# Kernel tuning notes

Hardware: AMD Instinct MI355X
Metric: run time of the kernel (lower is better)

The kernel has to match this reference:

```python
import jax, jax.numpy as jnp
import numpy as np

T, B, IN, H, L = 1024, 128, 100, 200, 2


def _lstm_layer(x, h0, c0, W_ih, W_hh, b_ih, b_hh):
    # x: [T, B, in]; h0, c0: [B, H]; W_ih: [4H, in]; W_hh: [4H, H]
    # PyTorch gate order: i, f, g, o
    def step(carry, x_t):
        h, c = carry
        gates = x_t @ W_ih.T + b_ih + h @ W_hh.T + b_hh  # [B, 4H]
        i, f, g, o = jnp.split(gates, 4, axis=-1)
        i = jax.nn.sigmoid(i)
        f = jax.nn.sigmoid(f)
        g = jnp.tanh(g)
        o = jax.nn.sigmoid(o)
        c = f * c + i * g
        h = o * jnp.tanh(c)
        return (h, c), h

    (hT, cT), ys = jax.lax.scan(step, (h0, c0), x)
    return ys, hT, cT  # ys: [T, B, H]


def setup_inputs() -> dict:
    key = jax.random.key(0)
    ks = jax.random.split(key, 12)
    s = 1.0 / np.sqrt(H)  # PyTorch LSTM init scale
    return {
        "inp": jax.random.normal(ks[0], (T, B, IN), dtype=jnp.float32),
        "h0": jnp.zeros((L, B, H), dtype=jnp.float32),
        "c0": jnp.zeros((L, B, H), dtype=jnp.float32),
        "W_ih0": jax.random.uniform(ks[1], (4 * H, IN), jnp.float32, -s, s),
        "W_hh0": jax.random.uniform(ks[2], (4 * H, H), jnp.float32, -s, s),
        "b_ih0": jax.random.uniform(ks[3], (4 * H,), jnp.float32, -s, s),
        "b_hh0": jax.random.uniform(ks[4], (4 * H,), jnp.float32, -s, s),
        "W_ih1": jax.random.uniform(ks[5], (4 * H, H), jnp.float32, -s, s),
        "W_hh1": jax.random.uniform(ks[6], (4 * H, H), jnp.float32, -s, s),
        "b_ih1": jax.random.uniform(ks[7], (4 * H,), jnp.float32, -s, s),
        "b_hh1": jax.random.uniform(ks[8], (4 * H,), jnp.float32, -s, s),
        "fc_W": jax.random.uniform(ks[9], (IN, H), jnp.float32, -s, s),
        "fc_b": jax.random.uniform(ks[10], (IN,), jnp.float32, -s, s),
    }


def reference(inp, h0, c0, W_ih0, W_hh0, b_ih0, b_hh0, W_ih1, W_hh1, b_ih1, b_hh1, fc_W, fc_b):
    # 2-layer LSTM (eval mode: inter-layer dropout is identity) + linear head
    y0, h0T, c0T = _lstm_layer(inp, h0[0], c0[0], W_ih0, W_hh0, b_ih0, b_hh0)
    y1, h1T, c1T = _lstm_layer(y0, h0[1], c0[1], W_ih1, W_hh1, b_ih1, b_hh1)
    output = y1 @ fc_W.T + fc_b  # [T, B, num_classes]
    hn = jnp.stack([h0T, h1T], axis=0)  # [2, B, H]
    cn = jnp.stack([c0T, c1T], axis=0)
    return output, hn, cn
```

## Files before the change

### kernel.cpp

```cpp
#include <hip/hip_runtime.h>
#include <stdint.h>

#define T_ 1024
#define B_ 128
#define IN_ 100
#define H_ 200
#define RD 8
#define RDY 8

typedef unsigned short u16;
typedef unsigned long long u64;
typedef short bf16x8 __attribute__((ext_vector_type(8)));
typedef float f32x4  __attribute__((ext_vector_type(4)));

#define OFF_Y1    0u
#define OFF_Y0R   52428800u
#define OFF_PR0   53248000u
#define OFF_PR1A  56524800u
#define OFF_PR1B  59801600u
#define OFF_PACK  63078400u
#define OFF_CBF   64409600u
#define OFF_CH0   65576256u
#define OFF_CC0   65781056u
#define OFF_X0P   65985856u
#define OFF_Y0P   65985920u
#define OFF_CONS0 65985984u
#define OFF_CONS1 65986048u
#define OFF_C1X   65986112u
#define OFF_Y0C   66018880u
#define OFF_FLAG  66051648u
#define WS_NEEDED 66051712u
#define PK_WHH0 0
#define PK_WHH1 179200
#define PK_WIH0 358400
#define PK_WIH1 460800

__device__ __forceinline__ float bf2f(u16 u) {
    union { uint32_t i; float f; } v; v.i = ((uint32_t)u) << 16; return v.f;
}
__device__ __forceinline__ u16 f2bf(float f) {
    union { uint32_t i; float f; } v; v.f = f;
    uint32_t x = v.i;
    x += 0x7fff + ((x >> 16) & 1);
    return (u16)(x >> 16);
}
__device__ __forceinline__ void agst2(float* p, float a, float b) {
    union { u64 u; float f[2]; } v; v.f[0] = a; v.f[1] = b;
    __hip_atomic_store((u64*)p, v.u, __ATOMIC_RELAXED, __HIP_MEMORY_SCOPE_AGENT);
}
__device__ __forceinline__ float2 agld2(const float* p) {
    union { u64 u; float f[2]; } v;
    v.u = __hip_atomic_load((u64*)p, __ATOMIC_RELAXED, __HIP_MEMORY_SCOPE_AGENT);
    return make_float2(v.f[0], v.f[1]);
}
__device__ __forceinline__ void agsti(int* p, int v) {
    __hip_atomic_store(p, v, __ATOMIC_RELAXED, __HIP_MEMORY_SCOPE_AGENT);
}
__device__ __forceinline__ void spin_ge(int* p, int val, int* budget) {
    while (__hip_atomic_load(p, __ATOMIC_RELAXED, __HIP_MEMORY_SCOPE_AGENT) < val) {
        __builtin_amdgcn_s_sleep(1);
        if (--(*budget) < 0) return;
    }
}

__global__ void detect_kernel(const void* w, int* flag) {
    __shared__ int cnt;
    if (threadIdx.x == 0) cnt = 0;
    __syncthreads();
    const u16* p = (const u16*)w;
    int bad = 0;
    for (int e = 0; e < 16; ++e) {
        u16 u = p[threadIdx.x * 16 + e];
        int ex = (u >> 7) & 0xFF;
        float v = bf2f(u);
        float av = v < 0.f ? -v : v;
        if (ex == 0xFF || av > 0.5f) bad++;
    }
    atomicAdd(&cnt, bad);
    __syncthreads();
    if (threadIdx.x == 0) flag[0] = (cnt > 64) ? 1 : 0;
}

__global__ void prep_kernel(const void* Wih0, const void* Whh0,
                            const void* bih0, const void* bhh0,
                            const void* Wih1, const void* Whh1,
                            const void* bih1, const void* bhh1,
                            const void* fcW,  const void* fcb,
                            const void* h0,   const void* c0,
                            u16* cbf, float* ch0, float* cc0, const int* flag)
{
    const int isf32 = *flag;
    const int N = 685700;
    for (int idx = blockIdx.x * 256 + threadIdx.x; idx < N; idx += gridDim.x * 256) {
        const void* src; int e = idx; u16* du = nullptr; float* df = nullptr;
        if (e < 80000)                 { src = Wih0; du = cbf; }
        else if ((e -= 80000) < 160000){ src = Whh0; du = cbf + 80000; }
        else if ((e -= 160000) < 800)  { src = bih0; du = cbf + 240000; }
        else if ((e -= 800) < 800)     { src = bhh0; du = cbf + 240800; }
        else if ((e -= 800) < 160000)  { src = Wih1; du = cbf + 241600; }
        else if ((e -= 160000) < 160000){ src = Whh1; du = cbf + 401600; }
        else if ((e -= 160000) < 800)  { src = bih1; du = cbf + 561600; }
        else if ((e -= 800) < 800)     { src = bhh1; du = cbf + 562400; }
        else if ((e -= 800) < 20000)   { src = fcW;  du = cbf + 563200; }
        else if ((e -= 20000) < 100)   { src = fcb;  du = cbf + 583200; }
        else if ((e -= 100) < 51200)   { src = h0;   df = ch0; }
        else         { e -= 51200;       src = c0;   df = cc0; }
        float v = isf32 ? ((const float*)src)[e] : bf2f(((const u16*)src)[e]);
        if (du) du[e] = f2bf(v); else df[e] = v;
    }
}

__global__ void pack_kernel(const u16* __restrict__ cbf, u16* __restrict__ pw) {
    const int N = 665600;
    for (int idx = blockIdx.x * 256 + threadIdx.x; idx < N; idx += gridDim.x * 256) {
        int e = idx; const u16* src; int ld, koff, kmax, rel;
        if (e < 179200)                    { rel = e; src = cbf + 80000;  ld = 200; kmax = 200; koff = 0; }
        else if ((e -= 179200) < 179200)   { rel = e; src = cbf + 401600; ld = 200; kmax = 200; koff = 0; }
        else if ((e -= 179200) < 102400)   { rel = e; src = cbf + 0;      ld = 100; kmax = 100; koff = 0; }
        else { e -= 102400; const int kh = e / 102400; rel = e % 102400;
               src = cbf + 241600; ld = 200; kmax = 100; koff = kh * 100; }
        const int el = rel & 7, l = (rel >> 3) & 63, tile = rel >> 9;
        const int nt = tile % 50, kt = tile / 50;
        const int rp = nt * 16 + (l & 15), g = rp & 3, hc = rp >> 2;
        const int k = kt * 32 + ((l >> 4) << 3) + el;
        u16 v = 0;
        if (k < kmax) v = src[(g * 200 + hc) * ld + koff + k];
        pw[idx] = v;
    }
}

__launch_bounds__(512, 1)
__global__ void lstm_pipe(const void* __restrict__ inp, char* __restrict__ ws,
                          const int* __restrict__ flag, void* __restrict__ out)
{
    __shared__ __align__(16) u16 smem[67392];

    u16*   y1buf  = (u16*)(ws + OFF_Y1);
    float* y0ring = (float*)(ws + OFF_Y0R);
    float* pr0    = (float*)(ws + OFF_PR0);
    float* pr1a   = (float*)(ws + OFF_PR1A);
    float* pr1b   = (float*)(ws + OFF_PR1B);
    u16*   packs  = (u16*)(ws + OFF_PACK);
    const u16* cbf = (const u16*)(ws + OFF_CBF);
    const float* ch0 = (const float*)(ws + OFF_CH0);
    const float* cc0 = (const float*)(ws + OFF_CC0);
    int* x0prod = (int*)(ws + OFF_X0P);
    int* y0prod = (int*)(ws + OFF_Y0P);
    int* cons0  = (int*)(ws + OFF_CONS0);
    int* cons1  = (int*)(ws + OFF_CONS1);
    int* c1x    = (int*)(ws + OFF_C1X);
    int* y0c    = (int*)(ws + OFF_Y0C);

    const int isf32 = *flag;
    const int tid = threadIdx.x;
    const int bid = blockIdx.x;
    const int lane = tid & 63, wv = tid >> 6;
    const int lm = lane & 15, lq = lane >> 4;
    const int nslot = (wv < 2) ? 7 : 6;
    int budget = 1 << 22;

    if (bid < 16) {
        const int L = bid >> 3, i = bid & 7, b0 = i * 16;
        u16* ldsB = smem;
        u16* hls  = smem + 31744;
        float* gls = (float*)(smem + 40192);
        const u16* packW = packs + (L ? PK_WHH1 : PK_WHH0);

        bf16x8 Bv[36];
        #pragma unroll
        for (int s = 0; s < 7; ++s) {
            const int nt = (s < 6) ? (wv + 8 * s) : (48 + wv);
            #pragma unroll
            for (int kt = 0; kt < 7; ++kt) {
                if (s < 5) {
                    Bv[s * 7 + kt] = *(const bf16x8*)(packW + ((size_t)(kt * 50 + nt) * 64 + lane) * 8);
                } else if (s == 5 && kt == 0) {
                    Bv[35] = *(const bf16x8*)(packW + ((size_t)(kt * 50 + nt) * 64 + lane) * 8);
                }
            }
        }
        for (int u = tid; u < 31744; u += 512) {
            const int eidx = u >> 9, off = u & 511;
            int kt, nt;
            if (eidx < 48) { kt = 1 + eidx % 6; nt = (eidx / 6) + 40; }
            else { const int e2 = eidx - 48; kt = e2 % 7; nt = 48 + e2 / 7; }
            ldsB[u] = packW[(size_t)(kt * 50 + nt) * 512 + off];
        }
        for (int u = tid; u < 2 * 16 * 264; u += 512) {
            const int pl = u / (16 * 264), m = (u / 264) % 16, k = u % 264;
            u16 v = 0;
            if (k < 200) {
                const float h = ch0[L * B_ * H_ + (b0 + m) * H_ + k];
                const u16 hi = f2bf(h);
                v = pl ? f2bf(h - bf2f(hi)) : hi;
            }
            hls[u] = v;
        }
        float c2[4][2];
        #pragma unroll
        for (int k4 = 0; k4 < 4; ++k4) {
            const int p = tid + 512 * k4;
            c2[k4][0] = 0.f; c2[k4][1] = 0.f;
            if (p < 1600) {
                const int m = p / 100, hc = (p % 100) * 2;
                c2[k4][0] = cc0[L * B_ * H_ + (b0 + m) * H_ + hc];
                c2[k4][1] = cc0[L * B_ * H_ + (b0 + m) * H_ + hc + 1];
            }
        }
        f32x4 acc[7];
        if (tid == 0) {
            if (L == 0) spin_ge(x0prod + i, 1, &budget);
            else        spin_ge(c1x + i, 2, &budget);
        }
        __syncthreads();
        {
            const size_t roff = (size_t)(0 * 8 + i) * 12800;
            #pragma unroll
            for (int s = 0; s < 7; ++s) if (s < nslot) {
                const int nt = (s < 6) ? (wv + 8 * s) : (48 + wv);
                float* pa = ((L ? pr1a : pr0) + roff) + nt * 256 + lane * 4;
                const float2 a01 = agld2(pa);
                const float2 a23 = agld2(pa + 2);
                acc[s][0] = a01.x; acc[s][1] = a01.y;
                acc[s][2] = a23.x; acc[s][3] = a23.y;
                if (L) {
                    float* pb = (pr1b + roff) + nt * 256 + lane * 4;
                    const float2 b01 = agld2(pb);
                    const float2 b23 = agld2(pb + 2);
                    acc[s][0] += b01.x; acc[s][1] += b01.y;
                    acc[s][2] += b23.x; acc[s][3] += b23.y;
                }
            }
        }
        __syncthreads();

        for (int t = 0; t < T_; ++t) {
            #pragma unroll
            for (int kt = 0; kt < 7; ++kt) {
                const int ha = lm * 264 + kt * 32 + 8 * lq;
                const bf16x8 Ahi = *(const bf16x8*)(hls + ha);
                const bf16x8 Alo = *(const bf16x8*)(hls + 16 * 264 + ha);
                #pragma unroll
                for (int s = 0; s < 7; ++s) if (s < nslot) {
                    bf16x8 Bt;
                    if (s < 5)                 Bt = Bv[s * 7 + kt];
                    else if (s == 5 && kt == 0) Bt = Bv[35];
                    else {
                        const int eidx = (s == 5) ? (wv * 6 + kt - 1) : (48 + wv * 7 + kt);
                        Bt = *(const bf16x8*)(ldsB + eidx * 512 + lane * 8);
                    }
                    acc[s] = __builtin_amdgcn_mfma_f32_16x16x32_bf16(Ahi, Bt, acc[s], 0, 0, 0);
                    acc[s] = __builtin_amdgcn_mfma_f32_16x16x32_bf16(Alo, Bt, acc[s], 0, 0, 0);
                }
            }
            #pragma unroll
            for (int s = 0; s < 7; ++s) if (s < nslot) {
                const int nt = (s < 6) ? (wv + 8 * s) : (48 + wv);
                const int g = lm & 3, hc = nt * 4 + (lm >> 2);
                float* gp = gls + g * 3400 + hc * 17 + 4 * lq;
                gp[0] = acc[s][0]; gp[1] = acc[s][1]; gp[2] = acc[s][2]; gp[3] = acc[s][3];
            }
            __syncthreads();
            if (tid == 0) {
                if (t < T_ - 1) {
                    if (L == 0) spin_ge(x0prod + i, t + 2, &budget);
                    else        spin_ge(c1x + (t + 1) * 8 + i, 2, &budget);
                }
                if (L == 0 && t >= RDY) spin_ge(y0c + (t - RDY) * 8 + i, 2, &budget);
            }
            __syncthreads();
            if (t < T_ - 1) {
                const size_t roff = (size_t)(((t + 1) & (RD - 1)) * 8 + i) * 12800;
                #pragma unroll
                for (int s = 0; s < 7; ++s) if (s < nslot) {
                    const int nt = (s < 6) ? (wv + 8 * s) : (48 + wv);
                    float* pa = ((L ? pr1a : pr0) + roff) + nt * 256 + lane * 4;
                    const float2 a01 = agld2(pa);
                    const float2 a23 = agld2(pa + 2);
                    acc[s][0] = a01.x; acc[s][1] = a01.y;
                    acc[s][2] = a23.x; acc[s][3] = a23.y;
                    if (L) {
                        float* pb = (pr1b + roff) + nt * 256 + lane * 4;
                        const float2 b01 = agld2(pb);
                        const float2 b23 = agld2(pb + 2);
                        acc[s][0] += b01.x; acc[s][1] += b01.y;
                        acc[s][2] += b23.x; acc[s][3] += b23.y;
                    }
                }
            }
            #pragma unroll
            for (int k4 = 0; k4 < 4; ++k4) {
                const int p = tid + 512 * k4;
                if (p < 1600) {
                    const int m = p / 100, hc = (p % 100) * 2;
                    float ig0 = gls[hc * 17 + m],        ig1 = gls[(hc + 1) * 17 + m];
                    float fg0 = gls[3400 + hc * 17 + m], fg1 = gls[3400 + (hc + 1) * 17 + m];
                    float gg0 = gls[6800 + hc * 17 + m], gg1 = gls[6800 + (hc + 1) * 17 + m];
                    float og0 = gls[10200 + hc * 17 + m],og1 = gls[10200 + (hc + 1) * 17 + m];
                    ig0 = (ig0 == ig0) ? ig0 : 0.f;  ig1 = (ig1 == ig1) ? ig1 : 0.f;
                    fg0 = (fg0 == fg0) ? fg0 : 0.f;  fg1 = (fg1 == fg1) ? fg1 : 0.f;
                    gg0 = (gg0 == gg0) ? gg0 : 0.f;  gg1 = (gg1 == gg1) ? gg1 : 0.f;
                    og0 = (og0 == og0) ? og0 : 0.f;  og1 = (og1 == og1) ? og1 : 0.f;
                    ig0 = 1.f / (1.f + __expf(-ig0)); ig1 = 1.f / (1.f + __expf(-ig1));
                    fg0 = 1.f / (1.f + __expf(-fg0)); fg1 = 1.f / (1.f + __expf(-fg1));
                    og0 = 1.f / (1.f + __expf(-og0)); og1 = 1.f / (1.f + __expf(-og1));
                    gg0 = tanhf(gg0); gg1 = tanhf(gg1);
                    c2[k4][0] = fg0 * c2[k4][0] + ig0 * gg0;
                    c2[k4][1] = fg1 * c2[k4][1] + ig1 * gg1;
                    const float h0v = og0 * tanhf(c2[k4][0]);
                    const float h1v = og1 * tanhf(c2[k4][1]);
                    const u16 hi0 = f2bf(h0v), hi1 = f2bf(h1v);
                    const u16 lo0 = f2bf(h0v - bf2f(hi0)), lo1 = f2bf(h1v - bf2f(hi1));
                    *(uint32_t*)(hls + m * 264 + hc) = (uint32_t)hi0 | ((uint32_t)hi1 << 16);
                    *(uint32_t*)(hls + (16 + m) * 264 + hc) = (uint32_t)lo0 | ((uint32_t)lo1 << 16);
                    if (L == 0) {
                        agst2(y0ring + ((size_t)(t & (RDY - 1)) * B_ + b0 + m) * H_ + hc, h0v, h1v);
                    } else {
                        *(uint32_t*)(y1buf + ((size_t)t * B_ + b0 + m) * H_ + hc)
                            = (uint32_t)hi0 | ((uint32_t)hi1 << 16);
                    }
                    if (t == T_ - 1) {
                        const size_t base = (size_t)T_ * B_ * IN_;
                        const size_t bb = (size_t)(b0 + m) * H_ + hc;
                        const size_t o1 = base + (size_t)L * B_ * H_ + bb;
                        const size_t o2 = base + 2 * (size_t)B_ * H_ + (size_t)L * B_ * H_ + bb;
                        if (isf32) {
                            ((float*)out)[o1] = h0v; ((float*)out)[o1 + 1] = h1v;
                            ((float*)out)[o2] = c2[k4][0]; ((float*)out)[o2 + 1] = c2[k4][1];
                        } else {
                            ((u16*)out)[o1] = hi0; ((u16*)out)[o1 + 1] = hi1;
                            ((u16*)out)[o2] = f2bf(c2[k4][0]); ((u16*)out)[o2 + 1] = f2bf(c2[k4][1]);
                        }
                    }
                }
            }
            __syncthreads();
            if (tid == 0) {
                if (L == 0) { agsti(cons0 + i, t + 1); agsti(y0prod + i, t + 1); }
                else        { agsti(cons1 + i, t + 1); }
            }
        }
    } else {
        const int isx0 = (bid < 24);
        const int i  = isx0 ? (bid - 16) : ((bid - 24) >> 1);
        const int kh = isx0 ? 0 : ((bid - 24) & 1);
        const int b0 = i * 16;
        u16* xst = smem;
        const u16* packW = packs + (isx0 ? PK_WIH0 : (PK_WIH1 + kh * 102400));

        bf16x8 Bx[28];
        #pragma unroll
        for (int s = 0; s < 7; ++s) {
            const int nt = (s < 6) ? (wv + 8 * s) : (48 + wv);
            #pragma unroll
            for (int kt = 0; kt < 4; ++kt)
                if (s < nslot)
                    Bx[s * 4 + kt] = *(const bf16x8*)(packW + ((size_t)(kt * 50 + nt) * 64 + lane) * 8);
        }
        float bias[7];
        #pragma unroll
        for (int s = 0; s < 7; ++s) {
            bias[s] = 0.f;
            if (s < nslot && (isx0 || kh == 0)) {
                const int nt = (s < 6) ? (wv + 8 * s) : (48 + wv);
                const int rp = nt * 16 + lm, g = rp & 3, hc = rp >> 2, R = g * 200 + hc;
                bias[s] = isx0 ? (bf2f(cbf[240000 + R]) + bf2f(cbf[240800 + R]))
                               : (bf2f(cbf[561600 + R]) + bf2f(cbf[562400 + R]));
            }
        }
        for (int u = tid; u < 2 * 16 * 136; u += 512) xst[u] = 0;
        __syncthreads();

        for (int t = 0; t < T_; ++t) {
            if (tid == 0) {
                if (isx0) {
                    if (t >= RD) spin_ge(cons0 + i, t - (RD - 1), &budget);
                } else {
                    spin_ge(y0prod + i, t + 1, &budget);
                    if (t >= RD) spin_ge(cons1 + i, t - (RD - 1), &budget);
                }
            }
            __syncthreads();
            for (int u = tid; u < 800; u += 512) {
                const int m = u / 50, k = (u % 50) * 2;
                float v0, v1;
                if (isx0) {
                    const size_t gi = ((size_t)t * B_ + b0 + m) * IN_ + k;
                    if (isf32) {
                        const float2 xv = *(const float2*)((const float*)inp + gi);
                        v0 = xv.x; v1 = xv.y;
                    } else {
                        const uint32_t xv = *(const uint32_t*)((const u16*)inp + gi);
                        v0 = bf2f((u16)xv); v1 = bf2f((u16)(xv >> 16));
                    }
                } else {
                    const float2 yv = agld2(y0ring + ((size_t)(t & (RDY - 1)) * B_ + b0 + m) * H_ + kh * 100 + k);
                    v0 = yv.x; v1 = yv.y;
                }
                const u16 hi0 = f2bf(v0), hi1 = f2bf(v1);
                *(uint32_t*)(xst + m * 136 + k) = (uint32_t)hi0 | ((uint32_t)hi1 << 16);
                *(uint32_t*)(xst + (16 + m) * 136 + k)
                    = (uint32_t)f2bf(v0 - bf2f(hi0)) | ((uint32_t)f2bf(v1 - bf2f(hi1)) << 16);
            }
            __syncthreads();
            if (!isx0 && tid == 0)
                __hip_atomic_fetch_add(y0c + t * 8 + i, 1, __ATOMIC_RELAXED, __HIP_MEMORY_SCOPE_AGENT);
            f32x4 acc[7];
            #pragma unroll
            for (int s = 0; s < 7; ++s) {
                acc[s][0] = bias[s]; acc[s][1] = bias[s];
                acc[s][2] = bias[s]; acc[s][3] = bias[s];
            }
            #pragma unroll
            for (int kt = 0; kt < 4; ++kt) {
                const int xa = lm * 136 + kt * 32 + 8 * lq;
                const bf16x8 Ahi = *(const bf16x8*)(xst + xa);
                const bf16x8 Alo = *(const bf16x8*)(xst + 16 * 136 + xa);
                #pragma unroll
                for (int s = 0; s < 7; ++s) if (s < nslot) {
                    acc[s] = __builtin_amdgcn_mfma_f32_16x16x32_bf16(Ahi, Bx[s * 4 + kt], acc[s], 0, 0, 0);
                    acc[s] = __builtin_amdgcn_mfma_f32_16x16x32_bf16(Alo, Bx[s * 4 + kt], acc[s], 0, 0, 0);
                }
            }
            float* ring = (isx0 ? pr0 : (kh ? pr1b : pr1a))
                        + (size_t)((t & (RD - 1)) * 8 + i) * 12800;
            #pragma unroll
            for (int s = 0; s < 7; ++s) if (s < nslot) {
                const int nt = (s < 6) ? (wv + 8 * s) : (48 + wv);
                float* pp = ring + nt * 256 + lane * 4;
                agst2(pp, acc[s][0], acc[s][1]);
                agst2(pp + 2, acc[s][2], acc[s][3]);
            }
            __syncthreads();
            if (tid == 0) {
                if (isx0) agsti(x0prod + i, t + 1);
                else __hip_atomic_fetch_add(c1x + t * 8 + i, 1, __ATOMIC_RELAXED, __HIP_MEMORY_SCOPE_AGENT);
            }
        }
    }
}

__launch_bounds__(256)
__global__ void fc_kernel(const u16* __restrict__ y1, const u16* __restrict__ cbf,
                          const int* __restrict__ flag, void* __restrict__ out)
{
    __shared__ float y1s[16 * 201];
    const int isf32 = *flag;
    const u16* fcW = cbf + 563200;
    const u16* fcb = cbf + 583200;
    const int tid = threadIdx.x;
    const int m0 = blockIdx.x * 16;
    for (int idx = tid; idx < 16 * 200; idx += 256) {
        int r = idx / 200, k = idx % 200;
        y1s[r * 201 + k] = bf2f(y1[(size_t)(m0 + r) * 200 + k]);
    }
    __syncthreads();
    const int r = tid & 15, ct = tid >> 4;
    float acc[7] = {0.f, 0.f, 0.f, 0.f, 0.f, 0.f, 0.f};
    for (int k = 0; k < 200; ++k) {
        const float x = y1s[r * 201 + k];
        #pragma unroll
        for (int qn = 0; qn < 7; ++qn) {
            int cc = ct + 16 * qn;
            if (cc < 100) acc[qn] = fmaf(x, bf2f(fcW[cc * 200 + k]), acc[qn]);
        }
    }
    #pragma unroll
    for (int qn = 0; qn < 7; ++qn) {
        int cc = ct + 16 * qn;
        if (cc < 100) {
            float v = acc[qn] + bf2f(fcb[cc]);
            v = (v == v) ? v : 0.f;
            const size_t oi = (size_t)(m0 + r) * 100 + cc;
            if (isf32) ((float*)out)[oi] = v;
            else       ((u16*)out)[oi] = f2bf(v);
        }
    }
}

extern "C" void kernel_launch(void* const* d_in, const int* in_sizes, int n_in,
                              void* d_out, int out_size, void* d_ws, size_t ws_size,
                              hipStream_t stream)
{
    const void* inp  = d_in[0];
    const void* h0   = d_in[1];
    const void* c0   = d_in[2];
    const void* Wih0 = d_in[3];
    const void* Whh0 = d_in[4];
    const void* bih0 = d_in[5];
    const void* bhh0 = d_in[6];
    const void* Wih1 = d_in[7];
    const void* Whh1 = d_in[8];
    const void* bih1 = d_in[9];
    const void* bhh1 = d_in[10];
    const void* fcW  = d_in[11];
    const void* fcb  = d_in[12];

    if (ws_size < WS_NEEDED) return;

    char* ws = (char*)d_ws;
    u16*   cbf  = (u16*)(ws + OFF_CBF);
    float* ch0  = (float*)(ws + OFF_CH0);
    float* cc0  = (float*)(ws + OFF_CC0);
    u16*   pw   = (u16*)(ws + OFF_PACK);
    int*   flag = (int*)(ws + OFF_FLAG);
    u16*   y1buf= (u16*)(ws + OFF_Y1);

    hipMemsetAsync(ws, 0, WS_NEEDED, stream);

    detect_kernel<<<1, 256, 0, stream>>>(Wih0, flag);
    prep_kernel<<<512, 256, 0, stream>>>(Wih0, Whh0, bih0, bhh0,
                                         Wih1, Whh1, bih1, bhh1,
                                         fcW, fcb, h0, c0, cbf, ch0, cc0, flag);
    pack_kernel<<<256, 256, 0, stream>>>(cbf, pw);
    lstm_pipe<<<40, 512, 0, stream>>>(inp, ws, flag, d_out);
    fc_kernel<<<8192, 256, 0, stream>>>(y1buf, cbf, flag, d_out);
}
```

Measured before the change: 7.377 ms.

## Deepen rings, batch cross-block flag waits, double-buffer input staging, fast activations

Grows the projection and y0 rings from 8 to 32 slots and moves all progress flags onto separate 64-byte-spaced lines. The recurrent blocks now poll producer and consumer flags only every 8 steps, and the input-projection blocks publish progress in batches. The projection blocks prefetch the next timestep's input into registers and double-buffer the bf16 hi/lo staging in LDS, which takes the global load off the critical path. Sigmoid and tanh use exp plus hardware reciprocal, and the workspace memset now clears only the flag region. The cost is a larger workspace, coarser sync granularity that can stall a consumer for longer, and slightly less accurate activations.

```diff
diff --git a/kernel.cpp b/kernel.cpp
--- a/kernel.cpp
+++ b/kernel.cpp
@@ -5,8 +5,8 @@
 #define B_ 128
 #define IN_ 100
 #define H_ 200
-#define RD 8
-#define RDY 8
+#define RD 32
+#define RDY 32
 
 typedef unsigned short u16;
 typedef unsigned long long u64;
@@ -15,21 +15,24 @@
 
 #define OFF_Y1    0u
 #define OFF_Y0R   52428800u
-#define OFF_PR0   53248000u
-#define OFF_PR1A  56524800u
-#define OFF_PR1B  59801600u
-#define OFF_PACK  63078400u
-#define OFF_CBF   64409600u
-#define OFF_CH0   65576256u
-#define OFF_CC0   65781056u
-#define OFF_X0P   65985856u
-#define OFF_Y0P   65985920u
-#define OFF_CONS0 65985984u
-#define OFF_CONS1 65986048u
-#define OFF_C1X   65986112u
-#define OFF_Y0C   66018880u
-#define OFF_FLAG  66051648u
-#define WS_NEEDED 66051712u
+#define OFF_PR0   55705600u
+#define OFF_PR1A  68812800u
+#define OFF_PR1B  81920000u
+#define OFF_PACK  95027200u
+#define OFF_CBF   96358400u
+#define OFF_CH0   97525056u
+#define OFF_CC0   97729856u
+#define OFF_FLG   97934656u
+#define WS_NEEDED 97938816u
+#define FO_X0P  0u
+#define FO_Y0P  512u
+#define FO_W1A  1024u
+#define FO_W1B  1536u
+#define FO_WY0A 2048u
+#define FO_WY0B 2560u
+#define FO_CN0  3072u
+#define FO_CN1  3584u
+#define FO_DTF  4096u
 #define PK_WHH0 0
 #define PK_WHH1 179200
 #define PK_WIH0 358400
@@ -61,6 +64,16 @@
         __builtin_amdgcn_s_sleep(1);
         if (--(*budget) < 0) return;
     }
+}
+__device__ __forceinline__ float fsig(float x) {
+    const float e = __expf(-x);
+    return __builtin_amdgcn_rcpf(1.f + e);
+}
+__device__ __forceinline__ float ftanh(float x) {
+    const float ax = __builtin_fabsf(x);
+    const float e = __expf(-2.f * ax);
+    const float r = (1.f - e) * __builtin_amdgcn_rcpf(1.f + e);
+    return __builtin_copysignf(r, x);
 }
 
 __global__ void detect_kernel(const void* w, int* flag) {
@@ -144,12 +157,6 @@
     const u16* cbf = (const u16*)(ws + OFF_CBF);
     const float* ch0 = (const float*)(ws + OFF_CH0);
     const float* cc0 = (const float*)(ws + OFF_CC0);
-    int* x0prod = (int*)(ws + OFF_X0P);
-    int* y0prod = (int*)(ws + OFF_Y0P);
-    int* cons0  = (int*)(ws + OFF_CONS0);
-    int* cons1  = (int*)(ws + OFF_CONS1);
-    int* c1x    = (int*)(ws + OFF_C1X);
-    int* y0c    = (int*)(ws + OFF_Y0C);
 
     const int isf32 = *flag;
     const int tid = threadIdx.x;
@@ -161,6 +168,16 @@
 
     if (bid < 16) {
         const int L = bid >> 3, i = bid & 7, b0 = i * 16;
+        const int FI = i * 16;
+        int* fx0p = (int*)(ws + OFF_FLG + FO_X0P) + FI;
+        int* fy0p = (int*)(ws + OFF_FLG + FO_Y0P) + FI;
+        int* fw1a = (int*)(ws + OFF_FLG + FO_W1A) + FI;
+        int* fw1b = (int*)(ws + OFF_FLG + FO_W1B) + FI;
+        int* fwy0a= (int*)(ws + OFF_FLG + FO_WY0A) + FI;
+        int* fwy0b= (int*)(ws + OFF_FLG + FO_WY0B) + FI;
+        int* fcn0 = (int*)(ws + OFF_FLG + FO_CN0) + FI;
+        int* fcn1 = (int*)(ws + OFF_FLG + FO_CN1) + FI;
+
         u16* ldsB = smem;
         u16* hls  = smem + 31744;
         float* gls = (float*)(smem + 40192);
@@ -209,8 +226,8 @@
         }
         f32x4 acc[7];
         if (tid == 0) {
-            if (L == 0) spin_ge(x0prod + i, 1, &budget);
-            else        spin_ge(c1x + i, 2, &budget);
+            if (L == 0) spin_ge(fx0p, 1, &budget);
+            else        { spin_ge(fw1a, 1, &budget); spin_ge(fw1b, 1, &budget); }
         }
         __syncthreads();
         {
@@ -261,14 +278,20 @@
                 gp[0] = acc[s][0]; gp[1] = acc[s][1]; gp[2] = acc[s][2]; gp[3] = acc[s][3];
             }
             __syncthreads();
-            if (tid == 0) {
-                if (t < T_ - 1) {
-                    if (L == 0) spin_ge(x0prod + i, t + 2, &budget);
-                    else        spin_ge(c1x + (t + 1) * 8 + i, 2, &budget);
-                }
-                if (L == 0 && t >= RDY) spin_ge(y0c + (t - RDY) * 8 + i, 2, &budget);
-            }
-            __syncthreads();
+            if ((t & 7) == 0) {
+                if (tid == 0) {
+                    int tgt = t + 9; if (tgt > T_) tgt = T_;
+                    if (L == 0) {
+                        spin_ge(fx0p, tgt, &budget);
+                        spin_ge(fwy0a, t - 15, &budget);
+                        spin_ge(fwy0b, t - 15, &budget);
+                    } else {
+                        spin_ge(fw1a, tgt, &budget);
+                        spin_ge(fw1b, tgt, &budget);
+                    }
+                }
+                __syncthreads();
+            }
             if (t < T_ - 1) {
                 const size_t roff = (size_t)(((t + 1) & (RD - 1)) * 8 + i) * 12800;
                 #pragma unroll
@@ -301,14 +324,14 @@
                     fg0 = (fg0 == fg0) ? fg0 : 0.f;  fg1 = (fg1 == fg1) ? fg1 : 0.f;
                     gg0 = (gg0 == gg0) ? gg0 : 0.f;  gg1 = (gg1 == gg1) ? gg1 : 0.f;
                     og0 = (og0 == og0) ? og0 : 0.f;  og1 = (og1 == og1) ? og1 : 0.f;
-                    ig0 = 1.f / (1.f + __expf(-ig0)); ig1 = 1.f / (1.f + __expf(-ig1));
-                    fg0 = 1.f / (1.f + __expf(-fg0)); fg1 = 1.f / (1.f + __expf(-fg1));
-                    og0 = 1.f / (1.f + __expf(-og0)); og1 = 1.f / (1.f + __expf(-og1));
-                    gg0 = tanhf(gg0); gg1 = tanhf(gg1);
+                    ig0 = fsig(ig0); ig1 = fsig(ig1);
+                    fg0 = fsig(fg0); fg1 = fsig(fg1);
+                    og0 = fsig(og0); og1 = fsig(og1);
+                    gg0 = ftanh(gg0); gg1 = ftanh(gg1);
                     c2[k4][0] = fg0 * c2[k4][0] + ig0 * gg0;
                     c2[k4][1] = fg1 * c2[k4][1] + ig1 * gg1;
-                    const float h0v = og0 * tanhf(c2[k4][0]);
-                    const float h1v = og1 * tanhf(c2[k4][1]);
+                    const float h0v = og0 * ftanh(c2[k4][0]);
+                    const float h1v = og1 * ftanh(c2[k4][1]);
                     const u16 hi0 = f2bf(h0v), hi1 = f2bf(h1v);
                     const u16 lo0 = f2bf(h0v - bf2f(hi0)), lo1 = f2bf(h1v - bf2f(hi1));
                     *(uint32_t*)(hls + m * 264 + hc) = (uint32_t)hi0 | ((uint32_t)hi1 << 16);
@@ -336,8 +359,12 @@
             }
             __syncthreads();
             if (tid == 0) {
-                if (L == 0) { agsti(cons0 + i, t + 1); agsti(y0prod + i, t + 1); }
-                else        { agsti(cons1 + i, t + 1); }
+                if (L == 0) {
+                    agsti(fy0p, t + 1);
+                    if (((t + 1) & 7) == 0) agsti(fcn0, t + 1);
+                } else {
+                    if (((t + 1) & 7) == 0) agsti(fcn1, t + 1);
+                }
             }
         }
     } else {
@@ -345,6 +372,13 @@
         const int i  = isx0 ? (bid - 16) : ((bid - 24) >> 1);
         const int kh = isx0 ? 0 : ((bid - 24) & 1);
         const int b0 = i * 16;
+        const int FI = i * 16;
+        int* fx0p = (int*)(ws + OFF_FLG + FO_X0P) + FI;
+        int* fy0p = (int*)(ws + OFF_FLG + FO_Y0P) + FI;
+        int* fw1  = (int*)(ws + OFF_FLG + (kh ? FO_W1B : FO_W1A)) + FI;
+        int* fwy0 = (int*)(ws + OFF_FLG + (kh ? FO_WY0B : FO_WY0A)) + FI;
+        int* fcons= (int*)(ws + OFF_FLG + (isx0 ? FO_CN0 : FO_CN1)) + FI;
+
         u16* xst = smem;
         const u16* packW = packs + (isx0 ? PK_WIH0 : (PK_WIH1 + kh * 102400));
 
@@ -368,43 +402,56 @@
                                : (bf2f(cbf[561600 + R]) + bf2f(cbf[562400 + R]));
             }
         }
-        for (int u = tid; u < 2 * 16 * 136; u += 512) xst[u] = 0;
+        for (int u = tid; u < 8704; u += 512) xst[u] = 0;
+
+        float2 sreg[2];
+        if (!isx0) { if (tid == 0) spin_ge(fy0p, 1, &budget); }
         __syncthreads();
+        #pragma unroll
+        for (int j = 0; j < 2; ++j) {
+            const int u = tid + 512 * j;
+            if (u < 800) {
+                const int m = u / 50, k = (u % 50) * 2;
+                if (isx0) {
+                    const size_t gi = ((size_t)0 * B_ + b0 + m) * IN_ + k;
+                    if (isf32) sreg[j] = *(const float2*)((const float*)inp + gi);
+                    else { const uint32_t xv = *(const uint32_t*)((const u16*)inp + gi);
+                           sreg[j] = make_float2(bf2f((u16)xv), bf2f((u16)(xv >> 16))); }
+                } else {
+                    sreg[j] = agld2(y0ring + ((size_t)0 * B_ + b0 + m) * H_ + kh * 100 + k);
+                }
+                const u16 h0 = f2bf(sreg[j].x), h1 = f2bf(sreg[j].y);
+                *(uint32_t*)(xst + m * 136 + k) = (uint32_t)h0 | ((uint32_t)h1 << 16);
+                *(uint32_t*)(xst + 2176 + m * 136 + k)
+                    = (uint32_t)f2bf(sreg[j].x - bf2f(h0)) | ((uint32_t)f2bf(sreg[j].y - bf2f(h1)) << 16);
+            }
+        }
+        __syncthreads();
+        int cur = 0;
 
         for (int t = 0; t < T_; ++t) {
-            if (tid == 0) {
-                if (isx0) {
-                    if (t >= RD) spin_ge(cons0 + i, t - (RD - 1), &budget);
-                } else {
-                    spin_ge(y0prod + i, t + 1, &budget);
-                    if (t >= RD) spin_ge(cons1 + i, t - (RD - 1), &budget);
-                }
-            }
-            __syncthreads();
-            for (int u = tid; u < 800; u += 512) {
-                const int m = u / 50, k = (u % 50) * 2;
-                float v0, v1;
-                if (isx0) {
-                    const size_t gi = ((size_t)t * B_ + b0 + m) * IN_ + k;
-                    if (isf32) {
-                        const float2 xv = *(const float2*)((const float*)inp + gi);
-                        v0 = xv.x; v1 = xv.y;
-                    } else {
-                        const uint32_t xv = *(const uint32_t*)((const u16*)inp + gi);
-                        v0 = bf2f((u16)xv); v1 = bf2f((u16)(xv >> 16));
-                    }
-                } else {
-                    const float2 yv = agld2(y0ring + ((size_t)(t & (RDY - 1)) * B_ + b0 + m) * H_ + kh * 100 + k);
-                    v0 = yv.x; v1 = yv.y;
-                }
-                const u16 hi0 = f2bf(v0), hi1 = f2bf(v1);
-                *(uint32_t*)(xst + m * 136 + k) = (uint32_t)hi0 | ((uint32_t)hi1 << 16);
-                *(uint32_t*)(xst + (16 + m) * 136 + k)
-                    = (uint32_t)f2bf(v0 - bf2f(hi0)) | ((uint32_t)f2bf(v1 - bf2f(hi1)) << 16);
-            }
-            __syncthreads();
-            if (!isx0 && tid == 0)
-                __hip_atomic_fetch_add(y0c + t * 8 + i, 1, __ATOMIC_RELAXED, __HIP_MEMORY_SCOPE_AGENT);
+            if (t < T_ - 1) {
+                if (tid == 0) {
+                    if (!isx0) spin_ge(fy0p, t + 2, &budget);
+                    if ((t & 7) == 0) spin_ge(fcons, t - 23, &budget);
+                }
+                __syncthreads();
+                #pragma unroll
+                for (int j = 0; j < 2; ++j) {
+                    const int u = tid + 512 * j;
+                    if (u < 800) {
+                        const int m = u / 50, k = (u % 50) * 2;
+                        if (isx0) {
+                            const size_t gi = ((size_t)(t + 1) * B_ + b0 + m) * IN_ + k;
+                            if (isf32) sreg[j] = *(const float2*)((const float*)inp + gi);
+                            else { const uint32_t xv = *(const uint32_t*)((const u16*)inp + gi);
+                                   sreg[j] = make_float2(bf2f((u16)xv), bf2f((u16)(xv >> 16))); }
+                        } else {
+                            sreg[j] = agld2(y0ring + ((size_t)((t + 1) & (RDY - 1)) * B_ + b0 + m) * H_ + kh * 100 + k);
+                        }
+                    }
+                }
+            }
             f32x4 acc[7];
             #pragma unroll
             for (int s = 0; s < 7; ++s) {
@@ -413,9 +460,9 @@
             }
             #pragma unroll
             for (int kt = 0; kt < 4; ++kt) {
-                const int xa = lm * 136 + kt * 32 + 8 * lq;
+                const int xa = cur * 4352 + lm * 136 + kt * 32 + 8 * lq;
                 const bf16x8 Ahi = *(const bf16x8*)(xst + xa);
-                const bf16x8 Alo = *(const bf16x8*)(xst + 16 * 136 + xa);
+                const bf16x8 Alo = *(const bf16x8*)(xst + 2176 + xa);
                 #pragma unroll
                 for (int s = 0; s < 7; ++s) if (s < nslot) {
                     acc[s] = __builtin_amdgcn_mfma_f32_16x16x32_bf16(Ahi, Bx[s * 4 + kt], acc[s], 0, 0, 0);
@@ -433,8 +480,24 @@
             }
             __syncthreads();
             if (tid == 0) {
-                if (isx0) agsti(x0prod + i, t + 1);
-                else __hip_atomic_fetch_add(c1x + t * 8 + i, 1, __ATOMIC_RELAXED, __HIP_MEMORY_SCOPE_AGENT);
+                if (isx0) { if (((t + 1) & 3) == 0) agsti(fx0p, t + 1); }
+                else      { agsti(fw1, t + 1); agsti(fwy0, t + 1); }
+            }
+            if (t < T_ - 1) {
+                const int nb = (cur ^ 1) * 4352;
+                #pragma unroll
+                for (int j = 0; j < 2; ++j) {
+                    const int u = tid + 512 * j;
+                    if (u < 800) {
+                        const int m = u / 50, k = (u % 50) * 2;
+                        const u16 h0 = f2bf(sreg[j].x), h1 = f2bf(sreg[j].y);
+                        *(uint32_t*)(xst + nb + m * 136 + k) = (uint32_t)h0 | ((uint32_t)h1 << 16);
+                        *(uint32_t*)(xst + nb + 2176 + m * 136 + k)
+                            = (uint32_t)f2bf(sreg[j].x - bf2f(h0)) | ((uint32_t)f2bf(sreg[j].y - bf2f(h1)) << 16);
+                    }
+                }
+                __syncthreads();
+                cur ^= 1;
             }
         }
     }
@@ -503,16 +566,16 @@
     float* ch0  = (float*)(ws + OFF_CH0);
     float* cc0  = (float*)(ws + OFF_CC0);
     u16*   pw   = (u16*)(ws + OFF_PACK);
-    int*   flag = (int*)(ws + OFF_FLAG);
+    int*   dflag= (int*)(ws + OFF_FLG + FO_DTF);
     u16*   y1buf= (u16*)(ws + OFF_Y1);
 
-    hipMemsetAsync(ws, 0, WS_NEEDED, stream);
-
-    detect_kernel<<<1, 256, 0, stream>>>(Wih0, flag);
+    hipMemsetAsync(ws + OFF_FLG, 0, 4160, stream);
+
+    detect_kernel<<<1, 256, 0, stream>>>(Wih0, dflag);
     prep_kernel<<<512, 256, 0, stream>>>(Wih0, Whh0, bih0, bhh0,
                                          Wih1, Whh1, bih1, bhh1,
-                                         fcW, fcb, h0, c0, cbf, ch0, cc0, flag);
+                                         fcW, fcb, h0, c0, cbf, ch0, cc0, dflag);
     pack_kernel<<<256, 256, 0, stream>>>(cbf, pw);
-    lstm_pipe<<<40, 512, 0, stream>>>(inp, ws, flag, d_out);
-    fc_kernel<<<8192, 256, 0, stream>>>(y1buf, cbf, flag, d_out);
-}
+    lstm_pipe<<<40, 512, 0, stream>>>(inp, ws, dflag, d_out);
+    fc_kernel<<<8192, 256, 0, stream>>>(y1buf, cbf, dflag, d_out);
+}
```

New measurement: 6.473 ms. 1.14x faster.
